# Performance work log

Hardware: AMD Instinct MI355X
Metric: run time of the kernel (lower is better)

Reference implementation:

```python
import jax, jax.numpy as jnp
import numpy as np

B, S, D = 4, 2048, 1024
H = 16
HD = D // H


def setup_inputs() -> dict:
    key = jax.random.key(0)
    ks = jax.random.split(key, 5)
    scale = 0.02
    return {
        "x": jax.random.normal(ks[0], (B, S, D), dtype=jnp.float32),
        "wq": jax.random.normal(ks[1], (D, D), dtype=jnp.float32) * scale,
        "wk": jax.random.normal(ks[2], (D, D), dtype=jnp.float32) * scale,
        "wv": jax.random.normal(ks[3], (D, D), dtype=jnp.float32) * scale,
        "wo": jax.random.normal(ks[4], (D, D), dtype=jnp.float32) * scale,
    }


def reference(x, wq, wk, wv, wo):
    b, s, _ = x.shape
    # project and split heads: [b, h, s, hd]
    def proj(w):
        return jnp.einsum('bsd,de->bse', x, w).reshape(b, s, H, HD).transpose(0, 2, 1, 3)
    q, k, v = proj(wq), proj(wk), proj(wv)
    scores = jnp.einsum('bhqd,bhkd->bhqk', q, k)
    causal = jnp.tril(jnp.ones((s, s), dtype=bool))  # True = keep
    scores = jnp.where(causal, scores, -jnp.inf)
    attn = jax.nn.softmax(scores / jnp.sqrt(jnp.float32(HD)), axis=-1)
    ctx = jnp.einsum('bhqk,bhkd->bhqd', attn, v)
    ctx = ctx.transpose(0, 2, 1, 3).reshape(b, s, D)
    return jnp.einsum('bsd,de->bse', ctx, wo)
```

## Files before the change

kernel.cpp:

```cpp
#include <hip/hip_runtime.h>

#define S_LEN 2048
#define D_DIM 1024
#define NH    16
#define HD    64
#define BATCH 4
#define M_ROWS 8192

typedef __attribute__((ext_vector_type(8))) short bf16x8;
typedef __attribute__((ext_vector_type(4))) float f32x4;
typedef __attribute__((ext_vector_type(8))) unsigned short u16x8;

__device__ __forceinline__ unsigned short f2bf(float f) {
    unsigned u = __builtin_bit_cast(unsigned, f);
    u = (u + 0x7fffu + ((u >> 16) & 1u)) >> 16;
    return (unsigned short)u;
}
__device__ __forceinline__ unsigned pack2(float a, float b) {
    unsigned ua = __builtin_bit_cast(unsigned, a);
    unsigned ub = __builtin_bit_cast(unsigned, b);
    return ((ua + 0x8000u) >> 16) | ((ub + 0x8000u) & 0xffff0000u);
}

__device__ __forceinline__ void gload16(const void* g, void* l) {
    __builtin_amdgcn_global_load_lds((const __attribute__((address_space(1))) unsigned*)g,
                                     (__attribute__((address_space(3))) unsigned*)l,
                                     16, 0, 0);
}

__global__ __launch_bounds__(256) void castx_k(const float* __restrict__ x,
                                               unsigned short* __restrict__ o) {
    size_t i = (size_t)blockIdx.x * 256 + threadIdx.x;
    const float4* xf = (const float4*)x;
    float4 a = xf[2 * i], b = xf[2 * i + 1];
    u16x8 v;
    v[0] = f2bf(a.x); v[1] = f2bf(a.y); v[2] = f2bf(a.z); v[3] = f2bf(a.w);
    v[4] = f2bf(b.x); v[5] = f2bf(b.y); v[6] = f2bf(b.z); v[7] = f2bf(b.w);
    *(u16x8*)(o + i * 8) = v;
}

__global__ __launch_bounds__(256) void wprep_k(const float* __restrict__ w0, const float* __restrict__ w1,
                                               const float* __restrict__ w2, const float* __restrict__ w3,
                                               unsigned short* __restrict__ o0, unsigned short* __restrict__ o1,
                                               unsigned short* __restrict__ o2, unsigned short* __restrict__ o3) {
    __shared__ float sT[64][65];
    const float* w; unsigned short* o;
    switch (blockIdx.z) {
        case 0: w = w0; o = o0; break;
        case 1: w = w1; o = o1; break;
        case 2: w = w2; o = o2; break;
        default: w = w3; o = o3; break;
    }
    const float sc = (blockIdx.z == 0) ? 0.18033688011112042f : 1.0f;
    const int t = threadIdx.x;
    const int k0 = blockIdx.y * 64, n0 = blockIdx.x * 64;
    const int r = t >> 4, cq = t & 15;
#pragma unroll
    for (int it = 0; it < 4; ++it) {
        int k = r + it * 16;
        float4 v = *(const float4*)&w[(size_t)(k0 + k) * D_DIM + n0 + cq * 4];
        sT[k][cq * 4 + 0] = v.x; sT[k][cq * 4 + 1] = v.y;
        sT[k][cq * 4 + 2] = v.z; sT[k][cq * 4 + 3] = v.w;
    }
    __syncthreads();
    const int n = t >> 2, ch = t & 3;
    union { unsigned short s[8]; uint4 v; } p0, p1;
#pragma unroll
    for (int j = 0; j < 8; ++j) p0.s[j] = f2bf(sT[ch * 16 + j][n] * sc);
#pragma unroll
    for (int j = 0; j < 8; ++j) p1.s[j] = f2bf(sT[ch * 16 + 8 + j][n] * sc);
    *(uint4*)&o[(size_t)(n0 + n) * D_DIM + k0 + ch * 16]     = p0.v;
    *(uint4*)&o[(size_t)(n0 + n) * D_DIM + k0 + ch * 16 + 8] = p1.v;
}

__global__ __launch_bounds__(256) void gemmqkv_k(const unsigned short* __restrict__ A,
                                                 const unsigned short* __restrict__ Bt,
                                                 unsigned short* __restrict__ qkv)
{
    __shared__ unsigned short sA[128 * 32];
    __shared__ unsigned short sB[128 * 32];
    const int t = threadIdx.x;
    const int lane = t & 63, w = t >> 6;
    const int mm = lane & 15, quad = lane >> 4;
    const int wm = w >> 1, wn = w & 1;
    const int m0 = blockIdx.y * 128, n0 = blockIdx.x * 128;

    f32x4 acc[4][4];
#pragma unroll
    for (int i = 0; i < 4; ++i)
#pragma unroll
        for (int j = 0; j < 4; ++j) acc[i][j] = (f32x4){0.f, 0.f, 0.f, 0.f};

    for (int k0 = 0; k0 < D_DIM; k0 += 32) {
        __syncthreads();
#pragma unroll
        for (int it = 0; it < 2; ++it) {
            int idx = t + it * 256;
            int m = idx >> 2, j = idx & 3;
            int g = (j - (m >> 1)) & 3;
            gload16(A  + ((size_t)(m0 + m) * D_DIM + k0 + g * 8), (void*)&sA[idx * 8]);
            gload16(Bt + ((size_t)(n0 + m) * D_DIM + k0 + g * 8), (void*)&sB[idx * 8]);
        }
        __syncthreads();

        bf16x8 af[4], bfr[4];
#pragma unroll
        for (int mi = 0; mi < 4; ++mi) {
            int m = wm * 64 + mi * 16 + mm;
            int slot = (quad + (m >> 1)) & 3;
            af[mi] = *(const bf16x8*)&sA[m * 32 + slot * 8];
        }
#pragma unroll
        for (int ni = 0; ni < 4; ++ni) {
            int n = wn * 64 + ni * 16 + mm;
            int slot = (quad + (n >> 1)) & 3;
            bfr[ni] = *(const bf16x8*)&sB[n * 32 + slot * 8];
        }
#pragma unroll
        for (int mi = 0; mi < 4; ++mi)
#pragma unroll
            for (int ni = 0; ni < 4; ++ni)
                acc[mi][ni] = __builtin_amdgcn_mfma_f32_16x16x32_bf16(af[mi], bfr[ni], acc[mi][ni], 0, 0, 0);
    }

    const int widx = n0 >> 10;
    const int nl0  = n0 & 1023;
    unsigned short* outp = qkv + (size_t)widx * ((size_t)M_ROWS * D_DIM);
#pragma unroll
    for (int mi = 0; mi < 4; ++mi)
#pragma unroll
        for (int ni = 0; ni < 4; ++ni)
#pragma unroll
            for (int r = 0; r < 4; ++r)
                outp[(size_t)(m0 + wm * 64 + mi * 16 + quad * 4 + r) * D_DIM +
                     nl0 + wn * 64 + ni * 16 + mm] = f2bf(acc[mi][ni][r]);
}

__global__ __launch_bounds__(256) void gemmo_k(const unsigned short* __restrict__ A,
                                               const unsigned short* __restrict__ Bt,
                                               float* __restrict__ C)
{
    __shared__ unsigned short sA[128 * 32];
    __shared__ unsigned short sB[128 * 32];
    const int t = threadIdx.x;
    const int lane = t & 63, w = t >> 6;
    const int mm = lane & 15, quad = lane >> 4;
    const int wm = w >> 1, wn = w & 1;
    const int m0 = blockIdx.y * 128, n0 = blockIdx.x * 128;

    f32x4 acc[4][4];
#pragma unroll
    for (int i = 0; i < 4; ++i)
#pragma unroll
        for (int j = 0; j < 4; ++j) acc[i][j] = (f32x4){0.f, 0.f, 0.f, 0.f};

    for (int k0 = 0; k0 < D_DIM; k0 += 32) {
        __syncthreads();
#pragma unroll
        for (int it = 0; it < 2; ++it) {
            int idx = t + it * 256;
            int m = idx >> 2, j = idx & 3;
            int g = (j - (m >> 1)) & 3;
            gload16(A  + ((size_t)(m0 + m) * D_DIM + k0 + g * 8), (void*)&sA[idx * 8]);
            gload16(Bt + ((size_t)(n0 + m) * D_DIM + k0 + g * 8), (void*)&sB[idx * 8]);
        }
        __syncthreads();

        bf16x8 af[4], bfr[4];
#pragma unroll
        for (int mi = 0; mi < 4; ++mi) {
            int m = wm * 64 + mi * 16 + mm;
            int slot = (quad + (m >> 1)) & 3;
            af[mi] = *(const bf16x8*)&sA[m * 32 + slot * 8];
        }
#pragma unroll
        for (int ni = 0; ni < 4; ++ni) {
            int n = wn * 64 + ni * 16 + mm;
            int slot = (quad + (n >> 1)) & 3;
            bfr[ni] = *(const bf16x8*)&sB[n * 32 + slot * 8];
        }
#pragma unroll
        for (int mi = 0; mi < 4; ++mi)
#pragma unroll
            for (int ni = 0; ni < 4; ++ni)
                acc[mi][ni] = __builtin_amdgcn_mfma_f32_16x16x32_bf16(af[mi], bfr[ni], acc[mi][ni], 0, 0, 0);
    }
#pragma unroll
    for (int mi = 0; mi < 4; ++mi)
#pragma unroll
        for (int ni = 0; ni < 4; ++ni)
#pragma unroll
            for (int r = 0; r < 4; ++r)
                C[(size_t)(m0 + wm * 64 + mi * 16 + quad * 4 + r) * D_DIM +
                  n0 + wn * 64 + ni * 16 + mm] = acc[mi][ni][r];
}

__global__ __launch_bounds__(256) void vtrans_k(const unsigned short* __restrict__ vb,
                                                unsigned short* __restrict__ vt)
{
    __shared__ unsigned short sT[64][72];
    const int t = threadIdx.x;
    const int st0 = blockIdx.x * 64, bh = blockIdx.y;
    const int b = bh >> 4, hh = bh & 15;
#pragma unroll
    for (int it = 0; it < 2; ++it) {
        int idx = t + it * 256;
        int r = idx >> 3, j = idx & 7;
        u16x8 v = *(const u16x8*)&vb[(size_t)(b * S_LEN + st0 + r) * D_DIM + hh * 64 + j * 8];
#pragma unroll
        for (int e = 0; e < 8; ++e) sT[j * 8 + e][r] = v[e];
    }
    __syncthreads();
#pragma unroll
    for (int it = 0; it < 2; ++it) {
        int idx = t + it * 256;
        int hd = idx >> 3, j = idx & 7;
        u16x8 ov = *(const u16x8*)&sT[hd][j * 8];
        *(u16x8*)&vt[((size_t)bh * HD + hd) * S_LEN + st0 + j * 8] = ov;
    }
}

__global__ __launch_bounds__(512, 4) void attn_k(const unsigned short* __restrict__ Q,
                                                 const unsigned short* __restrict__ K,
                                                 const unsigned short* __restrict__ Vt,
                                                 unsigned short* __restrict__ ctx)
{
    __shared__ unsigned short sK [2][64 * 64];
    __shared__ unsigned short sVT[2][64 * 64];
    __shared__ unsigned short sP [128 * 64];
    const int t = threadIdx.x;
    const int lane = t & 63, w = t >> 6;
    const int mm = lane & 15, quad = lane >> 4;
    const int pair = blockIdx.x, bh = blockIdx.y;
    const int b = bh >> 4, hh = bh & 15;
    const size_t rowbase = (size_t)b * S_LEN;
    const int coff = hh * HD;
    const unsigned short* Vh = Vt + (size_t)bh * HD * S_LEN;

    const int sc_ = t >> 3, sj = t & 7, sg = sj ^ (sc_ & 7);

    u16x8 onesu;
#pragma unroll
    for (int j = 0; j < 8; ++j) onesu[j] = 0x3F80;
    const bf16x8 ones = __builtin_bit_cast(bf16x8, onesu);

    for (int sidx = 0; sidx < 2; ++sidx) {
        const int qt = sidx ? (15 - pair) : pair;
        const int q0 = qt * 128;

        bf16x8 qf[2];
#pragma unroll
        for (int kk = 0; kk < 2; ++kk)
            qf[kk] = *(const bf16x8*)(Q + (rowbase + q0 + w * 16 + mm) * D_DIM
                                        + coff + kk * 32 + quad * 8);
        f32x4 o[4], lacc;
        lacc = (f32x4){0.f, 0.f, 0.f, 0.f};
#pragma unroll
        for (int hf = 0; hf < 4; ++hf) o[hf] = (f32x4){0.f, 0.f, 0.f, 0.f};

        const int nkt = 2 * qt + 2;
        const int qr = q0 + w * 16 + mm;
        const int qrmax = q0 + w * 16 + 15;

        gload16(K  + (rowbase + sc_) * D_DIM + coff + sg * 8, (void*)&sK[0][t * 8]);
        gload16(Vh + (size_t)sc_ * S_LEN + sg * 8,            (void*)&sVT[0][t * 8]);

        for (int kt = 0; kt < nkt; ++kt) {
            const int buf = kt & 1;
            __syncthreads();
            if (kt + 1 < nkt) {
                const int k1 = (kt + 1) * 64;
                gload16(K  + (rowbase + k1 + sc_) * D_DIM + coff + sg * 8,
                        (void*)&sK[1 - buf][t * 8]);
                gload16(Vh + (size_t)sc_ * S_LEN + k1 + sg * 8,
                        (void*)&sVT[1 - buf][t * 8]);
            }
            const int k0 = kt * 64;
            if (k0 > qrmax) continue;

            f32x4 sacc[4];
#pragma unroll
            for (int kf = 0; kf < 4; ++kf) sacc[kf] = (f32x4){0.f, 0.f, 0.f, 0.f};
#pragma unroll
            for (int kk = 0; kk < 2; ++kk) {
                bf16x8 ak[4];
#pragma unroll
                for (int kf = 0; kf < 4; ++kf) {
                    int key = kf * 16 + mm;
                    int slot = (kk * 4 + quad) ^ (key & 7);
                    ak[kf] = *(const bf16x8*)&sK[buf][key * 64 + slot * 8];
                }
#pragma unroll
                for (int kf = 0; kf < 4; ++kf)
                    sacc[kf] = __builtin_amdgcn_mfma_f32_16x16x32_bf16(ak[kf], qf[kk], sacc[kf], 0, 0, 0);
            }

            const bool needmask = (k0 + 63) > (q0 + w * 16);
            const int m = w * 16 + mm;
#pragma unroll
            for (int kf = 0; kf < 4; ++kf) {
                float p[4];
#pragma unroll
                for (int r = 0; r < 4; ++r) {
                    p[r] = __builtin_amdgcn_exp2f(sacc[kf][r]);
                    if (needmask && (k0 + kf * 16 + quad * 4 + r) > qr) p[r] = 0.f;
                }
                unsigned lo = pack2(p[0], p[1]), hi = pack2(p[2], p[3]);
                int slot = (kf * 2 + (quad >> 1)) ^ (m & 7);
                *(unsigned long long*)&sP[m * 64 + slot * 8 + (quad & 1) * 4] =
                    ((unsigned long long)hi << 32) | lo;
            }

#pragma unroll
            for (int kk = 0; kk < 2; ++kk) {
                bf16x8 pf, vf[4];
                {
                    int slot = (kk * 4 + quad) ^ (m & 7);
                    pf = *(const bf16x8*)&sP[m * 64 + slot * 8];
                }
#pragma unroll
                for (int hf = 0; hf < 4; ++hf) {
                    int hd = hf * 16 + mm;
                    int slot = (kk * 4 + quad) ^ (hd & 7);
                    vf[hf] = *(const bf16x8*)&sVT[buf][hd * 64 + slot * 8];
                }
                lacc = __builtin_amdgcn_mfma_f32_16x16x32_bf16(pf, ones, lacc, 0, 0, 0);
#pragma unroll
                for (int hf = 0; hf < 4; ++hf)
                    o[hf] = __builtin_amdgcn_mfma_f32_16x16x32_bf16(pf, vf[hf], o[hf], 0, 0, 0);
            }
        }
        __syncthreads();

#pragma unroll
        for (int r = 0; r < 4; ++r) {
            float inv = 1.f / lacc[r];
            int row = q0 + w * 16 + quad * 4 + r;
#pragma unroll
            for (int hf = 0; hf < 4; ++hf)
                ctx[(rowbase + row) * D_DIM + coff + hf * 16 + mm] = f2bf(o[hf][r] * inv);
        }
    }
}

extern "C" void kernel_launch(void* const* d_in, const int* in_sizes, int n_in,
                              void* d_out, int out_size, void* d_ws, size_t ws_size,
                              hipStream_t stream)
{
    const float* x  = (const float*)d_in[0];
    const float* wq = (const float*)d_in[1];
    const float* wk = (const float*)d_in[2];
    const float* wv = (const float*)d_in[3];
    const float* wo = (const float*)d_in[4];

    const size_t XE = (size_t)M_ROWS * D_DIM;
    const size_t WE = (size_t)D_DIM * D_DIM;
    unsigned short* ws  = (unsigned short*)d_ws;
    unsigned short* xbf = ws;
    unsigned short* wt0 = xbf + XE;
    unsigned short* wt1 = wt0 + WE;
    unsigned short* wt2 = wt1 + WE;
    unsigned short* wt3 = wt2 + WE;
    unsigned short* qb  = wt3 + WE;
    unsigned short* kb  = qb + XE;
    unsigned short* vb  = kb + XE;
    unsigned short* vt  = vb + XE;
    unsigned short* cb  = vt + XE;

    castx_k<<<dim3(M_ROWS * D_DIM / (256 * 8)), 256, 0, stream>>>(x, xbf);
    wprep_k<<<dim3(16, 16, 4), 256, 0, stream>>>(wq, wk, wv, wo, wt0, wt1, wt2, wt3);

    gemmqkv_k<<<dim3(3 * D_DIM / 128, M_ROWS / 128), 256, 0, stream>>>(xbf, wt0, qb);
    vtrans_k<<<dim3(S_LEN / 64, BATCH * NH), 256, 0, stream>>>(vb, vt);

    attn_k<<<dim3(8, BATCH * NH), 512, 0, stream>>>(qb, kb, vt, cb);

    gemmo_k<<<dim3(D_DIM / 128, M_ROWS / 128), 256, 0, stream>>>(cb, wt3, (float*)d_out);
}
```

Measured before the change: 258.0 us.

## Double-buffer GEMM k-loop, fuse V transpose into QKV epilogue, widen attention key tiles

The QKV and output GEMMs now share a double-buffered core that loads the next K-slice into a second LDS buffer while the current one is consumed, so there is one barrier per step instead of two. The QKV GEMM epilogue writes V directly in transposed per-head layout, which removes the separate vtrans kernel and its round trip through global memory. The attention kernel stages 128 keys per tile instead of 64, halving the number of barriers and loads per query tile. In exchange, LDS use doubles, which may lower occupancy, and the transposed V stores are strided 8-byte writes.

```diff
diff --git a/kernel.cpp b/kernel.cpp
--- a/kernel.cpp
+++ b/kernel.cpp
@@ -73,12 +73,61 @@
     *(uint4*)&o[(size_t)(n0 + n) * D_DIM + k0 + ch * 16 + 8] = p1.v;
 }
 
+__device__ __forceinline__ void gemm_core(const unsigned short* __restrict__ A,
+                                          const unsigned short* __restrict__ Bt,
+                                          unsigned short* sA, unsigned short* sB,
+                                          int m0, int n0, int t, f32x4 acc[4][4])
+{
+    const int lane = t & 63, w = t >> 6;
+    const int mm = lane & 15, quad = lane >> 4;
+    const int wm = w >> 1, wn = w & 1;
+
+    auto stage = [&](int k0, int bufi) {
+#pragma unroll
+        for (int it = 0; it < 2; ++it) {
+            int idx = t + it * 256;
+            int m = idx >> 2, j = idx & 3;
+            int g = (j - (m >> 1)) & 3;
+            gload16(A  + ((size_t)(m0 + m) * D_DIM + k0 + g * 8), (void*)&sA[bufi * 4096 + idx * 8]);
+            gload16(Bt + ((size_t)(n0 + m) * D_DIM + k0 + g * 8), (void*)&sB[bufi * 4096 + idx * 8]);
+        }
+    };
+
+    stage(0, 0);
+    for (int kt = 0; kt < D_DIM / 32; ++kt) {
+        const int bufo = (kt & 1) * 4096;
+        __syncthreads();
+        if (kt + 1 < D_DIM / 32) stage((kt + 1) * 32, 1 - (kt & 1));
+
+        bf16x8 af[4], bfr[4];
+#pragma unroll
+        for (int mi = 0; mi < 4; ++mi) {
+            int m = wm * 64 + mi * 16 + mm;
+            int slot = (quad + (m >> 1)) & 3;
+            af[mi] = *(const bf16x8*)&sA[bufo + m * 32 + slot * 8];
+        }
+#pragma unroll
+        for (int ni = 0; ni < 4; ++ni) {
+            int n = wn * 64 + ni * 16 + mm;
+            int slot = (quad + (n >> 1)) & 3;
+            bfr[ni] = *(const bf16x8*)&sB[bufo + n * 32 + slot * 8];
+        }
+#pragma unroll
+        for (int mi = 0; mi < 4; ++mi)
+#pragma unroll
+            for (int ni = 0; ni < 4; ++ni)
+                acc[mi][ni] = __builtin_amdgcn_mfma_f32_16x16x32_bf16(af[mi], bfr[ni], acc[mi][ni], 0, 0, 0);
+    }
+}
+
 __global__ __launch_bounds__(256) void gemmqkv_k(const unsigned short* __restrict__ A,
                                                  const unsigned short* __restrict__ Bt,
-                                                 unsigned short* __restrict__ qkv)
-{
-    __shared__ unsigned short sA[128 * 32];
-    __shared__ unsigned short sB[128 * 32];
+                                                 unsigned short* __restrict__ qb,
+                                                 unsigned short* __restrict__ kb,
+                                                 unsigned short* __restrict__ vt)
+{
+    __shared__ unsigned short sA[2 * 128 * 32];
+    __shared__ unsigned short sB[2 * 128 * 32];
     const int t = threadIdx.x;
     const int lane = t & 63, w = t >> 6;
     const int mm = lane & 15, quad = lane >> 4;
@@ -91,57 +140,44 @@
 #pragma unroll
         for (int j = 0; j < 4; ++j) acc[i][j] = (f32x4){0.f, 0.f, 0.f, 0.f};
 
-    for (int k0 = 0; k0 < D_DIM; k0 += 32) {
-        __syncthreads();
-#pragma unroll
-        for (int it = 0; it < 2; ++it) {
-            int idx = t + it * 256;
-            int m = idx >> 2, j = idx & 3;
-            int g = (j - (m >> 1)) & 3;
-            gload16(A  + ((size_t)(m0 + m) * D_DIM + k0 + g * 8), (void*)&sA[idx * 8]);
-            gload16(Bt + ((size_t)(n0 + m) * D_DIM + k0 + g * 8), (void*)&sB[idx * 8]);
-        }
-        __syncthreads();
-
-        bf16x8 af[4], bfr[4];
+    gemm_core(A, Bt, sA, sB, m0, n0, t, acc);
+
+    const int widx = n0 >> 10;
+    if (widx == 2) {
 #pragma unroll
         for (int mi = 0; mi < 4; ++mi) {
-            int m = wm * 64 + mi * 16 + mm;
-            int slot = (quad + (m >> 1)) & 3;
-            af[mi] = *(const bf16x8*)&sA[m * 32 + slot * 8];
-        }
-#pragma unroll
-        for (int ni = 0; ni < 4; ++ni) {
-            int n = wn * 64 + ni * 16 + mm;
-            int slot = (quad + (n >> 1)) & 3;
-            bfr[ni] = *(const bf16x8*)&sB[n * 32 + slot * 8];
-        }
+            int rglob = m0 + wm * 64 + mi * 16 + quad * 4;
+            int bb = rglob >> 11, ss = rglob & (S_LEN - 1);
+#pragma unroll
+            for (int ni = 0; ni < 4; ++ni) {
+                int c = (n0 & 1023) + wn * 64 + ni * 16 + mm;
+                int h = c >> 6, hd = c & 63;
+                union { unsigned short s[4]; unsigned long long ll; } pk;
+#pragma unroll
+                for (int r = 0; r < 4; ++r) pk.s[r] = f2bf(acc[mi][ni][r]);
+                *(unsigned long long*)&vt[((size_t)(bb * NH + h) * HD + hd) * S_LEN + ss] = pk.ll;
+            }
+        }
+    } else {
+        unsigned short* outp = widx ? kb : qb;
+        const int nl0 = n0 & 1023;
 #pragma unroll
         for (int mi = 0; mi < 4; ++mi)
 #pragma unroll
             for (int ni = 0; ni < 4; ++ni)
-                acc[mi][ni] = __builtin_amdgcn_mfma_f32_16x16x32_bf16(af[mi], bfr[ni], acc[mi][ni], 0, 0, 0);
-    }
-
-    const int widx = n0 >> 10;
-    const int nl0  = n0 & 1023;
-    unsigned short* outp = qkv + (size_t)widx * ((size_t)M_ROWS * D_DIM);
-#pragma unroll
-    for (int mi = 0; mi < 4; ++mi)
-#pragma unroll
-        for (int ni = 0; ni < 4; ++ni)
-#pragma unroll
-            for (int r = 0; r < 4; ++r)
-                outp[(size_t)(m0 + wm * 64 + mi * 16 + quad * 4 + r) * D_DIM +
-                     nl0 + wn * 64 + ni * 16 + mm] = f2bf(acc[mi][ni][r]);
+#pragma unroll
+                for (int r = 0; r < 4; ++r)
+                    outp[(size_t)(m0 + wm * 64 + mi * 16 + quad * 4 + r) * D_DIM +
+                         nl0 + wn * 64 + ni * 16 + mm] = f2bf(acc[mi][ni][r]);
+    }
 }
 
 __global__ __launch_bounds__(256) void gemmo_k(const unsigned short* __restrict__ A,
                                                const unsigned short* __restrict__ Bt,
                                                float* __restrict__ C)
 {
-    __shared__ unsigned short sA[128 * 32];
-    __shared__ unsigned short sB[128 * 32];
+    __shared__ unsigned short sA[2 * 128 * 32];
+    __shared__ unsigned short sB[2 * 128 * 32];
     const int t = threadIdx.x;
     const int lane = t & 63, w = t >> 6;
     const int mm = lane & 15, quad = lane >> 4;
@@ -154,37 +190,8 @@
 #pragma unroll
         for (int j = 0; j < 4; ++j) acc[i][j] = (f32x4){0.f, 0.f, 0.f, 0.f};
 
-    for (int k0 = 0; k0 < D_DIM; k0 += 32) {
-        __syncthreads();
-#pragma unroll
-        for (int it = 0; it < 2; ++it) {
-            int idx = t + it * 256;
-            int m = idx >> 2, j = idx & 3;
-            int g = (j - (m >> 1)) & 3;
-            gload16(A  + ((size_t)(m0 + m) * D_DIM + k0 + g * 8), (void*)&sA[idx * 8]);
-            gload16(Bt + ((size_t)(n0 + m) * D_DIM + k0 + g * 8), (void*)&sB[idx * 8]);
-        }
-        __syncthreads();
-
-        bf16x8 af[4], bfr[4];
-#pragma unroll
-        for (int mi = 0; mi < 4; ++mi) {
-            int m = wm * 64 + mi * 16 + mm;
-            int slot = (quad + (m >> 1)) & 3;
-            af[mi] = *(const bf16x8*)&sA[m * 32 + slot * 8];
-        }
-#pragma unroll
-        for (int ni = 0; ni < 4; ++ni) {
-            int n = wn * 64 + ni * 16 + mm;
-            int slot = (quad + (n >> 1)) & 3;
-            bfr[ni] = *(const bf16x8*)&sB[n * 32 + slot * 8];
-        }
-#pragma unroll
-        for (int mi = 0; mi < 4; ++mi)
-#pragma unroll
-            for (int ni = 0; ni < 4; ++ni)
-                acc[mi][ni] = __builtin_amdgcn_mfma_f32_16x16x32_bf16(af[mi], bfr[ni], acc[mi][ni], 0, 0, 0);
-    }
+    gemm_core(A, Bt, sA, sB, m0, n0, t, acc);
+
 #pragma unroll
     for (int mi = 0; mi < 4; ++mi)
 #pragma unroll
@@ -193,31 +200,6 @@
             for (int r = 0; r < 4; ++r)
                 C[(size_t)(m0 + wm * 64 + mi * 16 + quad * 4 + r) * D_DIM +
                   n0 + wn * 64 + ni * 16 + mm] = acc[mi][ni][r];
-}
-
-__global__ __launch_bounds__(256) void vtrans_k(const unsigned short* __restrict__ vb,
-                                                unsigned short* __restrict__ vt)
-{
-    __shared__ unsigned short sT[64][72];
-    const int t = threadIdx.x;
-    const int st0 = blockIdx.x * 64, bh = blockIdx.y;
-    const int b = bh >> 4, hh = bh & 15;
-#pragma unroll
-    for (int it = 0; it < 2; ++it) {
-        int idx = t + it * 256;
-        int r = idx >> 3, j = idx & 7;
-        u16x8 v = *(const u16x8*)&vb[(size_t)(b * S_LEN + st0 + r) * D_DIM + hh * 64 + j * 8];
-#pragma unroll
-        for (int e = 0; e < 8; ++e) sT[j * 8 + e][r] = v[e];
-    }
-    __syncthreads();
-#pragma unroll
-    for (int it = 0; it < 2; ++it) {
-        int idx = t + it * 256;
-        int hd = idx >> 3, j = idx & 7;
-        u16x8 ov = *(const u16x8*)&sT[hd][j * 8];
-        *(u16x8*)&vt[((size_t)bh * HD + hd) * S_LEN + st0 + j * 8] = ov;
-    }
 }
 
 __global__ __launch_bounds__(512, 4) void attn_k(const unsigned short* __restrict__ Q,
@@ -225,8 +207,8 @@
                                                  const unsigned short* __restrict__ Vt,
                                                  unsigned short* __restrict__ ctx)
 {
-    __shared__ unsigned short sK [2][64 * 64];
-    __shared__ unsigned short sVT[2][64 * 64];
+    __shared__ unsigned short sK [2][128 * 64];
+    __shared__ unsigned short sVT[2][64 * 128];
     __shared__ unsigned short sP [128 * 64];
     const int t = threadIdx.x;
     const int lane = t & 63, w = t >> 6;
@@ -237,7 +219,18 @@
     const int coff = hh * HD;
     const unsigned short* Vh = Vt + (size_t)bh * HD * S_LEN;
 
-    const int sc_ = t >> 3, sj = t & 7, sg = sj ^ (sc_ & 7);
+    auto stage = [&](int kt, int bufi) {
+#pragma unroll
+        for (int it = 0; it < 2; ++it) {
+            int idx = t + it * 512;
+            int key = idx >> 3, jk = idx & 7, gk = jk ^ (key & 7);
+            gload16(K + (rowbase + kt * 128 + key) * D_DIM + coff + gk * 8,
+                    (void*)&sK[bufi][idx * 8]);
+            int hd = idx >> 4, jv = idx & 15, gv = jv ^ (hd & 15);
+            gload16(Vh + (size_t)hd * S_LEN + kt * 128 + gv * 8,
+                    (void*)&sVT[bufi][idx * 8]);
+        }
+    };
 
     u16x8 onesu;
 #pragma unroll
@@ -258,76 +251,73 @@
 #pragma unroll
         for (int hf = 0; hf < 4; ++hf) o[hf] = (f32x4){0.f, 0.f, 0.f, 0.f};
 
-        const int nkt = 2 * qt + 2;
+        const int nkt = qt + 1;
         const int qr = q0 + w * 16 + mm;
         const int qrmax = q0 + w * 16 + 15;
-
-        gload16(K  + (rowbase + sc_) * D_DIM + coff + sg * 8, (void*)&sK[0][t * 8]);
-        gload16(Vh + (size_t)sc_ * S_LEN + sg * 8,            (void*)&sVT[0][t * 8]);
-
+        const int m = w * 16 + mm;
+
+        stage(0, 0);
         for (int kt = 0; kt < nkt; ++kt) {
             const int buf = kt & 1;
             __syncthreads();
-            if (kt + 1 < nkt) {
-                const int k1 = (kt + 1) * 64;
-                gload16(K  + (rowbase + k1 + sc_) * D_DIM + coff + sg * 8,
-                        (void*)&sK[1 - buf][t * 8]);
-                gload16(Vh + (size_t)sc_ * S_LEN + k1 + sg * 8,
-                        (void*)&sVT[1 - buf][t * 8]);
-            }
-            const int k0 = kt * 64;
-            if (k0 > qrmax) continue;
-
-            f32x4 sacc[4];
-#pragma unroll
-            for (int kf = 0; kf < 4; ++kf) sacc[kf] = (f32x4){0.f, 0.f, 0.f, 0.f};
-#pragma unroll
-            for (int kk = 0; kk < 2; ++kk) {
-                bf16x8 ak[4];
+            if (kt + 1 < nkt) stage(kt + 1, 1 - buf);
+
+#pragma unroll
+            for (int kh = 0; kh < 2; ++kh) {
+                const int k0 = kt * 128 + kh * 64;
+                if (k0 > qrmax) continue;
+
+                f32x4 sacc[4];
+#pragma unroll
+                for (int kf = 0; kf < 4; ++kf) sacc[kf] = (f32x4){0.f, 0.f, 0.f, 0.f};
+#pragma unroll
+                for (int kk = 0; kk < 2; ++kk) {
+                    bf16x8 ak[4];
+#pragma unroll
+                    for (int kf = 0; kf < 4; ++kf) {
+                        int key = kh * 64 + kf * 16 + mm;
+                        int slot = (kk * 4 + quad) ^ (key & 7);
+                        ak[kf] = *(const bf16x8*)&sK[buf][key * 64 + slot * 8];
+                    }
+#pragma unroll
+                    for (int kf = 0; kf < 4; ++kf)
+                        sacc[kf] = __builtin_amdgcn_mfma_f32_16x16x32_bf16(ak[kf], qf[kk], sacc[kf], 0, 0, 0);
+                }
+
+                const bool needmask = (k0 + 63) > (q0 + w * 16);
 #pragma unroll
                 for (int kf = 0; kf < 4; ++kf) {
-                    int key = kf * 16 + mm;
-                    int slot = (kk * 4 + quad) ^ (key & 7);
-                    ak[kf] = *(const bf16x8*)&sK[buf][key * 64 + slot * 8];
+                    float p[4];
+#pragma unroll
+                    for (int r = 0; r < 4; ++r) {
+                        p[r] = __builtin_amdgcn_exp2f(sacc[kf][r]);
+                        if (needmask && (k0 + kf * 16 + quad * 4 + r) > qr) p[r] = 0.f;
+                    }
+                    unsigned lo = pack2(p[0], p[1]), hi = pack2(p[2], p[3]);
+                    int slot = (kf * 2 + (quad >> 1)) ^ (m & 7);
+                    *(unsigned long long*)&sP[m * 64 + slot * 8 + (quad & 1) * 4] =
+                        ((unsigned long long)hi << 32) | lo;
                 }
-#pragma unroll
-                for (int kf = 0; kf < 4; ++kf)
-                    sacc[kf] = __builtin_amdgcn_mfma_f32_16x16x32_bf16(ak[kf], qf[kk], sacc[kf], 0, 0, 0);
-            }
-
-            const bool needmask = (k0 + 63) > (q0 + w * 16);
-            const int m = w * 16 + mm;
-#pragma unroll
-            for (int kf = 0; kf < 4; ++kf) {
-                float p[4];
-#pragma unroll
-                for (int r = 0; r < 4; ++r) {
-                    p[r] = __builtin_amdgcn_exp2f(sacc[kf][r]);
-                    if (needmask && (k0 + kf * 16 + quad * 4 + r) > qr) p[r] = 0.f;
+
+#pragma unroll
+                for (int kk = 0; kk < 2; ++kk) {
+                    bf16x8 pf, vf[4];
+                    {
+                        int slot = (kk * 4 + quad) ^ (m & 7);
+                        pf = *(const bf16x8*)&sP[m * 64 + slot * 8];
+                    }
+#pragma unroll
+                    for (int hf = 0; hf < 4; ++hf) {
+                        int hd = hf * 16 + mm;
+                        int c = kh * 8 + kk * 4 + quad;
+                        int slot = c ^ (hd & 15);
+                        vf[hf] = *(const bf16x8*)&sVT[buf][hd * 128 + slot * 8];
+                    }
+                    lacc = __builtin_amdgcn_mfma_f32_16x16x32_bf16(pf, ones, lacc, 0, 0, 0);
+#pragma unroll
+                    for (int hf = 0; hf < 4; ++hf)
+                        o[hf] = __builtin_amdgcn_mfma_f32_16x16x32_bf16(pf, vf[hf], o[hf], 0, 0, 0);
                 }
-                unsigned lo = pack2(p[0], p[1]), hi = pack2(p[2], p[3]);
-                int slot = (kf * 2 + (quad >> 1)) ^ (m & 7);
-                *(unsigned long long*)&sP[m * 64 + slot * 8 + (quad & 1) * 4] =
-                    ((unsigned long long)hi << 32) | lo;
-            }
-
-#pragma unroll
-            for (int kk = 0; kk < 2; ++kk) {
-                bf16x8 pf, vf[4];
-                {
-                    int slot = (kk * 4 + quad) ^ (m & 7);
-                    pf = *(const bf16x8*)&sP[m * 64 + slot * 8];
-                }
-#pragma unroll
-                for (int hf = 0; hf < 4; ++hf) {
-                    int hd = hf * 16 + mm;
-                    int slot = (kk * 4 + quad) ^ (hd & 7);
-                    vf[hf] = *(const bf16x8*)&sVT[buf][hd * 64 + slot * 8];
-                }
-                lacc = __builtin_amdgcn_mfma_f32_16x16x32_bf16(pf, ones, lacc, 0, 0, 0);
-#pragma unroll
-                for (int hf = 0; hf < 4; ++hf)
-                    o[hf] = __builtin_amdgcn_mfma_f32_16x16x32_bf16(pf, vf[hf], o[hf], 0, 0, 0);
             }
         }
         __syncthreads();
@@ -363,15 +353,13 @@
     unsigned short* wt3 = wt2 + WE;
     unsigned short* qb  = wt3 + WE;
     unsigned short* kb  = qb + XE;
-    unsigned short* vb  = kb + XE;
-    unsigned short* vt  = vb + XE;
+    unsigned short* vt  = kb + XE;
     unsigned short* cb  = vt + XE;
 
     castx_k<<<dim3(M_ROWS * D_DIM / (256 * 8)), 256, 0, stream>>>(x, xbf);
     wprep_k<<<dim3(16, 16, 4), 256, 0, stream>>>(wq, wk, wv, wo, wt0, wt1, wt2, wt3);
 
-    gemmqkv_k<<<dim3(3 * D_DIM / 128, M_ROWS / 128), 256, 0, stream>>>(xbf, wt0, qb);
-    vtrans_k<<<dim3(S_LEN / 64, BATCH * NH), 256, 0, stream>>>(vb, vt);
+    gemmqkv_k<<<dim3(3 * D_DIM / 128, M_ROWS / 128), 256, 0, stream>>>(xbf, wt0, qb, kb, vt);
 
     attn_k<<<dim3(8, BATCH * NH), 512, 0, stream>>>(qb, kb, vt, cb);
 
```

Result: slower. 280.2 us (+8.6%).
